# Optimization experiments

Hardware: AMD Instinct MI355X
Metric: run time of the kernel (lower is better)

Reference implementation:

```python
import jax, jax.numpy as jnp
import numpy as np
from jax import lax

NUM_LAYERS = 2
H = 1024   # per-direction hidden = state_size / 2
IN = 768   # BERT hidden size == input_size
SEQ = 1024


def _init_params(key):
    ks = jax.random.split(key, 4 * NUM_LAYERS * 2)
    mk = lambda k, shape: jax.random.normal(k, shape, jnp.float32) * 0.02
    out = {}
    i = 0
    for d in ("fw", "bw"):
        for l in range(NUM_LAYERS):
            ins = IN if l == 0 else H
            out[f"{d}{l}_Wih"] = mk(ks[i], (4 * H, ins)); i += 1
            out[f"{d}{l}_Whh"] = mk(ks[i], (4 * H, H)); i += 1
            out[f"{d}{l}_bih"] = mk(ks[i], (4 * H,)); i += 1
            out[f"{d}{l}_bhh"] = mk(ks[i], (4 * H,)); i += 1
    return out


def setup_inputs() -> dict:
    key = jax.random.key(0)
    kx, kp = jax.random.split(key)
    inp = {"last_hidden": jax.random.normal(kx, (1, SEQ, IN), jnp.float32)}
    inp.update(_init_params(kp))
    return inp


def _run_direction(x, params):
    """x: [S, in_dim]; params: list of (Wih, Whh, bih, bhh) per layer.
    Stacked LSTMCells (torch gate order i,f,g,o), dropout_amount=0."""
    def step(carry, xt):
        new = []
        inp = xt
        for (h, c), (Wih, Whh, bih, bhh) in zip(carry, params):
            gates = Wih @ inp + bih + Whh @ h + bhh  # [4H]
            i, f, g, o = jnp.split(gates, 4)
            c = jax.nn.sigmoid(f) * c + jax.nn.sigmoid(i) * jnp.tanh(g)
            h = jax.nn.sigmoid(o) * jnp.tanh(c)
            new.append((h, c))
            inp = h
        return tuple(new), inp  # output = top layer h
    init = tuple((jnp.zeros((H,), x.dtype), jnp.zeros((H,), x.dtype)) for _ in params)
    final, outs = lax.scan(step, init, x)
    cs = jnp.stack([c for (_, c) in final])  # [L, H] final cell states
    hs = jnp.stack([h for (h, _) in final])  # [L, H] final hidden states
    return cs, hs, outs                      # outs: [S, H]


def reference(last_hidden, fw0_Wih, fw0_Whh, fw0_bih, fw0_bhh,
              fw1_Wih, fw1_Whh, fw1_bih, fw1_bhh,
              bw0_Wih, bw0_Whh, bw0_bih, bw0_bhh,
              bw1_Wih, bw1_Whh, bw1_bih, bw1_bhh):
    x = last_hidden[0]  # squeeze batch of 1 -> [S, IN]
    fw = [(fw0_Wih, fw0_Whh, fw0_bih, fw0_bhh), (fw1_Wih, fw1_Whh, fw1_bih, fw1_bhh)]
    bw = [(bw0_Wih, bw0_Whh, bw0_bih, bw0_bhh), (bw1_Wih, bw1_Whh, bw1_bih, bw1_bhh)]
    f_c, f_h, f_out = _run_direction(x, fw)
    b_c, b_h, b_out = _run_direction(x[::-1], bw)
    b_out = b_out[::-1]  # re-align backward outputs with token order
    cell_memories = jnp.concatenate([f_c, b_c], axis=1)      # [L, 2H]
    hidden_states = jnp.concatenate([f_h, b_h], axis=1)      # [L, 2H]
    final_outputs = jnp.concatenate([f_out, b_out], axis=1)  # [S, 2H]
    return cell_memories, hidden_states, final_outputs
```

## Files before the change

kernel.cpp:

```cpp
#include <hip/hip_runtime.h>

typedef unsigned int u32;
typedef unsigned short u16;
typedef unsigned long long u64;
typedef __attribute__((ext_vector_type(8))) short v8s;
typedef __attribute__((ext_vector_type(4))) float v4f;

#define VALIDMASK 0x0001000100010001ULL

__device__ __forceinline__ float bf2f(u16 v) { return __uint_as_float(((u32)v) << 16); }
__device__ __forceinline__ u16 f2bf(float f) {
    u32 u = __float_as_uint(f);
    return (u16)((u + 0x7fffu + ((u >> 16) & 1u)) >> 16);
}
__device__ __forceinline__ u32 f2bfo(float f) { return (__float_as_uint(f) >> 16) | 1u; }
__device__ __forceinline__ float sigf(float x) { return 1.0f / (1.0f + __expf(-x)); }
__device__ __forceinline__ float tanhfast(float x) {
    float e = __expf(2.0f * x);
    return 1.0f - 2.0f / (e + 1.0f);
}
__device__ __forceinline__ v8s pack8(v4f a, v4f b) {
    v8s r;
    r[0] = (short)f2bf(a[0]); r[1] = (short)f2bf(a[1]);
    r[2] = (short)f2bf(a[2]); r[3] = (short)f2bf(a[3]);
    r[4] = (short)f2bf(b[0]); r[5] = (short)f2bf(b[1]);
    r[6] = (short)f2bf(b[2]); r[7] = (short)f2bf(b[3]);
    return r;
}

__global__ __launch_bounds__(256) void gemm_ih(
    const float* __restrict__ A, const float* __restrict__ W,
    const float* __restrict__ bih, const float* __restrict__ bhh,
    u16* __restrict__ out, int K)
{
    __shared__ u16 As[128][40];
    __shared__ u16 Bs[128][40];
    const int tm = blockIdx.x, tn = blockIdx.y;
    const int tid = threadIdx.x;
    const int lane = tid & 63;
    const int wv = tid >> 6;
    const int wm = wv >> 1, wn = wv & 1;
    const int fr = lane & 15, fq = lane >> 4;

    v4f acc[4][4] = {};

    for (int kt = 0; kt < K; kt += 32) {
#pragma unroll
        for (int it = 0; it < 2; ++it) {
            int q = tid + it * 256;
            int r = q >> 2;
            int c8 = (q & 3) * 8;
            const float* pa = &A[(size_t)(tm * 128 + r) * K + kt + c8];
            const float* pw = &W[(size_t)(tn * 128 + r) * K + kt + c8];
            *(v8s*)&As[r][c8] = pack8(*(const v4f*)pa, *(const v4f*)(pa + 4));
            *(v8s*)&Bs[r][c8] = pack8(*(const v4f*)pw, *(const v4f*)(pw + 4));
        }
        __syncthreads();
        v8s af[4], bfr[4];
#pragma unroll
        for (int mi = 0; mi < 4; ++mi)
            af[mi] = *(const v8s*)&As[wm * 64 + mi * 16 + fr][fq * 8];
#pragma unroll
        for (int ni = 0; ni < 4; ++ni)
            bfr[ni] = *(const v8s*)&Bs[wn * 64 + ni * 16 + fr][fq * 8];
#pragma unroll
        for (int mi = 0; mi < 4; ++mi)
#pragma unroll
            for (int ni = 0; ni < 4; ++ni)
                acc[mi][ni] = __builtin_amdgcn_mfma_f32_16x16x32_bf16(af[mi], bfr[ni], acc[mi][ni], 0, 0, 0);
        __syncthreads();
    }

#pragma unroll
    for (int ni = 0; ni < 4; ++ni) {
        int col = tn * 128 + wn * 64 + ni * 16 + fr;
        float bias = bih[col] + bhh[col];
#pragma unroll
        for (int mi = 0; mi < 4; ++mi)
#pragma unroll
            for (int j = 0; j < 4; ++j) {
                int row = tm * 128 + wm * 64 + mi * 16 + fq * 4 + j;
                out[(size_t)row * 4096 + col] = f2bf(acc[mi][ni][j] + bias);
            }
    }
}

__global__ __launch_bounds__(64, 1) void lstm_fused(
    const float* __restrict__ fw0_Whh, const float* __restrict__ bw0_Whh,
    const float* __restrict__ fw1_Whh, const float* __restrict__ bw1_Whh,
    const float* __restrict__ fw1_Wih, const float* __restrict__ bw1_Wih,
    const float* __restrict__ fw1_bih, const float* __restrict__ fw1_bhh,
    const float* __restrict__ bw1_bih, const float* __restrict__ bw1_bhh,
    const u16*  __restrict__ precomp0,
    u64* htag0,
    u64* htag1,
    float* __restrict__ out)
{
    extern __shared__ char smem[];
    char* hA = smem + 65536;
    char* hB = smem + 65536 + 2048;
    float* gd = (float*)(smem + 65536 + 4096);

    const int lane = threadIdx.x;
    const int bid = blockIdx.x;
    const int role = bid >> 8;
    const int sub = bid & 255;
    const int d = sub >> 7;
    const int wg = sub & 127;
    const int e0 = wg << 3;

    const float* __restrict__ Whh =
        role ? (d ? bw1_Whh : fw1_Whh) : (d ? bw0_Whh : fw0_Whh);

    v8s awf0[32], awf1[32];
    {
        int r0 = lane & 15, r1 = r0 + 16;
        int kq = (lane >> 4) << 3;
        const float* q0 = &Whh[(size_t)((r0 >> 3) * 1024 + e0 + (r0 & 7)) * 1024 + kq];
        const float* q1 = &Whh[(size_t)((r1 >> 3) * 1024 + e0 + (r1 & 7)) * 1024 + kq];
#pragma unroll
        for (int c = 0; c < 32; ++c) {
            awf0[c] = pack8(*(const v4f*)(q0 + 32 * c), *(const v4f*)(q0 + 32 * c + 4));
            awf1[c] = pack8(*(const v4f*)(q1 + 32 * c), *(const v4f*)(q1 + 32 * c + 4));
        }
    }

    float bias_i = 0.f, bias_f = 0.f, bias_g = 0.f, bias_o = 0.f;
    if (role) {
        const float* __restrict__ Wih = d ? bw1_Wih : fw1_Wih;
        for (int i = 0; i < 64; ++i) {
            int q = lane + (i << 6);
            int row = q >> 7;
            int kb = (q & 127) << 4;
            const float* p = &Wih[(size_t)((row >> 3) * 1024 + e0 + (row & 7)) * 1024 + (kb >> 1)];
            int addr = (row << 11) + kb;
            addr ^= ((row & 7) << 4);
            *(v8s*)(smem + addr) = pack8(*(const v4f*)p, *(const v4f*)(p + 4));
        }
        if (lane < 8) {
            const float* bi = d ? bw1_bih : fw1_bih;
            const float* bh = d ? bw1_bhh : fw1_bhh;
            bias_i = bi[e0 + lane]        + bh[e0 + lane];
            bias_f = bi[1024 + e0 + lane] + bh[1024 + e0 + lane];
            bias_g = bi[2048 + e0 + lane] + bh[2048 + e0 + lane];
            bias_o = bi[3072 + e0 + lane] + bh[3072 + e0 + lane];
        }
    }

    u64* hown = (role ? htag1 : htag0) + (size_t)d * 1024 * 256;
    u64* hin  = htag0 + (size_t)d * 1024 * 256;
    float* cm_out = out + role * 2048;
    float* hs_out = out + 4096 + role * 2048;
    float* seq_out = out + 8192;

    float c_state = 0.0f;

    for (int s = 0; s < 1024; ++s) {
        v4f acc0 = {0.f, 0.f, 0.f, 0.f}, acc1 = {0.f, 0.f, 0.f, 0.f};

        u16 ri = 0, rf = 0, rg = 0, ro = 0;
        if (!role && lane < 8) {
            int sx = d ? (1023 - s) : s;
            const u16* pr = precomp0 + ((size_t)d * 1024 + sx) * 4096 + e0 + lane;
            ri = pr[0]; rf = pr[1024]; rg = pr[2048]; ro = pr[3072];
        }

        if (role) {
            u64* p = hin + (size_t)s * 256 + (lane << 2);
            u64 a, b, c2, d2;
            for (;;) {
                a  = __hip_atomic_load(&p[0], __ATOMIC_RELAXED, __HIP_MEMORY_SCOPE_AGENT);
                b  = __hip_atomic_load(&p[1], __ATOMIC_RELAXED, __HIP_MEMORY_SCOPE_AGENT);
                c2 = __hip_atomic_load(&p[2], __ATOMIC_RELAXED, __HIP_MEMORY_SCOPE_AGENT);
                d2 = __hip_atomic_load(&p[3], __ATOMIC_RELAXED, __HIP_MEMORY_SCOPE_AGENT);
                if ((((a & b) & (c2 & d2)) & VALIDMASK) == VALIDMASK) break;
                __builtin_amdgcn_s_sleep(1);
            }
            *(u64*)(hB + (lane << 5))      = a;
            *(u64*)(hB + (lane << 5) + 8)  = b;
            *(u64*)(hB + (lane << 5) + 16) = c2;
            *(u64*)(hB + (lane << 5) + 24) = d2;
            asm volatile("s_waitcnt lgkmcnt(0)" ::: "memory");
            int r0 = lane & 15;
            int sw = (r0 & 7) << 4;
#pragma unroll
            for (int c = 0; c < 32; ++c) {
                int kb = (c << 6) + ((lane >> 4) << 4);
                v8s bfr = *(const v8s*)(hB + kb);
                v8s a0 = *(const v8s*)(smem + (((r0 << 11) + kb) ^ sw));
                v8s a1 = *(const v8s*)(smem + ((((r0 + 16) << 11) + kb) ^ sw));
                acc0 = __builtin_amdgcn_mfma_f32_16x16x32_bf16(a0, bfr, acc0, 0, 0, 0);
                acc1 = __builtin_amdgcn_mfma_f32_16x16x32_bf16(a1, bfr, acc1, 0, 0, 0);
            }
        }

        if (s > 0) {
            u64* p = hown + (size_t)(s - 1) * 256 + (lane << 2);
            u64 a, b, c2, d2;
            for (;;) {
                a  = __hip_atomic_load(&p[0], __ATOMIC_RELAXED, __HIP_MEMORY_SCOPE_AGENT);
                b  = __hip_atomic_load(&p[1], __ATOMIC_RELAXED, __HIP_MEMORY_SCOPE_AGENT);
                c2 = __hip_atomic_load(&p[2], __ATOMIC_RELAXED, __HIP_MEMORY_SCOPE_AGENT);
                d2 = __hip_atomic_load(&p[3], __ATOMIC_RELAXED, __HIP_MEMORY_SCOPE_AGENT);
                if ((((a & b) & (c2 & d2)) & VALIDMASK) == VALIDMASK) break;
                __builtin_amdgcn_s_sleep(1);
            }
            *(u64*)(hA + (lane << 5))      = a;
            *(u64*)(hA + (lane << 5) + 8)  = b;
            *(u64*)(hA + (lane << 5) + 16) = c2;
            *(u64*)(hA + (lane << 5) + 24) = d2;
            asm volatile("s_waitcnt lgkmcnt(0)" ::: "memory");
#pragma unroll
            for (int c = 0; c < 32; ++c) {
                v8s bfr = *(const v8s*)(hA + (c << 6) + ((lane >> 4) << 4));
                acc0 = __builtin_amdgcn_mfma_f32_16x16x32_bf16(awf0[c], bfr, acc0, 0, 0, 0);
                acc1 = __builtin_amdgcn_mfma_f32_16x16x32_bf16(awf1[c], bfr, acc1, 0, 0, 0);
            }
        }

        if ((lane & 15) == 0) {
            int rbase = (lane >> 4) << 2;
            *(v4f*)&gd[rbase]      = acc0;
            *(v4f*)&gd[16 + rbase] = acc1;
        }
        asm volatile("s_waitcnt lgkmcnt(0)" ::: "memory");

        float h_new = 0.0f;
        if (lane < 8) {
            float Gi = gd[lane]      + (role ? bias_i : bf2f(ri));
            float Gf = gd[8 + lane]  + (role ? bias_f : bf2f(rf));
            float Gg = gd[16 + lane] + (role ? bias_g : bf2f(rg));
            float Go = gd[24 + lane] + (role ? bias_o : bf2f(ro));
            c_state = sigf(Gf) * c_state + sigf(Gi) * tanhfast(Gg);
            h_new = sigf(Go) * tanhfast(c_state);
        }

        u32 w0 = f2bfo(__shfl(h_new, (lane << 2)))     | (f2bfo(__shfl(h_new, (lane << 2) + 1)) << 16);
        u32 w1 = f2bfo(__shfl(h_new, (lane << 2) + 2)) | (f2bfo(__shfl(h_new, (lane << 2) + 3)) << 16);
        if (lane < 2) {
            u64 val = ((u64)w1 << 32) | w0;
            __hip_atomic_store(&hown[(size_t)s * 256 + (e0 >> 2) + lane], val,
                               __ATOMIC_RELAXED, __HIP_MEMORY_SCOPE_AGENT);
        }

        if (lane < 8) {
            if (role) {
                int rrow = d ? (1023 - s) : s;
                seq_out[(size_t)rrow * 2048 + d * 1024 + e0 + lane] = h_new;
            }
            if (s == 1023) {
                cm_out[d * 1024 + e0 + lane] = c_state;
                hs_out[d * 1024 + e0 + lane] = h_new;
            }
        }
    }
}

extern "C" void kernel_launch(void* const* d_in, const int* in_sizes, int n_in,
                              void* d_out, int out_size, void* d_ws, size_t ws_size,
                              hipStream_t stream) {
    (void)in_sizes; (void)n_in; (void)out_size; (void)ws_size;

    const float* x       = (const float*)d_in[0];
    const float* fw0_Wih = (const float*)d_in[1];
    const float* fw0_Whh = (const float*)d_in[2];
    const float* fw0_bih = (const float*)d_in[3];
    const float* fw0_bhh = (const float*)d_in[4];
    const float* fw1_Wih = (const float*)d_in[5];
    const float* fw1_Whh = (const float*)d_in[6];
    const float* fw1_bih = (const float*)d_in[7];
    const float* fw1_bhh = (const float*)d_in[8];
    const float* bw0_Wih = (const float*)d_in[9];
    const float* bw0_Whh = (const float*)d_in[10];
    const float* bw0_bih = (const float*)d_in[11];
    const float* bw0_bhh = (const float*)d_in[12];
    const float* bw1_Wih = (const float*)d_in[13];
    const float* bw1_Whh = (const float*)d_in[14];
    const float* bw1_bih = (const float*)d_in[15];
    const float* bw1_bhh = (const float*)d_in[16];

    char* ws = (char*)d_ws;
    u16* precomp = (u16*)ws;
    u64* htag0   = (u64*)(ws + (16 << 20));
    u64* htag1   = (u64*)(ws + (20 << 20));
    float* out   = (float*)d_out;

    hipMemsetAsync(htag0, 0, (size_t)8 << 20, stream);

    dim3 g(8, 32);
    gemm_ih<<<g, 256, 0, stream>>>(x, fw0_Wih, fw0_bih, fw0_bhh, precomp, 768);
    gemm_ih<<<g, 256, 0, stream>>>(x, bw0_Wih, bw0_bih, bw0_bhh,
                                   precomp + (size_t)1024 * 4096, 768);

    lstm_fused<<<512, 64, 69760, stream>>>(
        fw0_Whh, bw0_Whh, fw1_Whh, bw1_Whh, fw1_Wih, bw1_Wih,
        fw1_bih, fw1_bhh, bw1_bih, bw1_bhh,
        precomp, htag0, htag1, out);
}
```

Before: 3.430 ms.

## Relayout LDS weight tile, coalesce h polling, split MFMA accumulators, raise priority

Rearranges the layer-1 input-weight tile in shared memory into a fragment-major, conflict-free layout so each lane reads contiguous 16-byte chunks without the XOR swizzle. The hidden-state polling loads change from four consecutive words per lane to strided words across lanes, which coalesces the global reads, and the LDS staging is changed to match. The MFMA chains are split into two independent accumulator pairs to shorten dependency chains. s_setprio raises wave priority during the matmul section. The risk is that the new LDS layout introduces bank conflicts, and the extra accumulator registers add pressure next to the 64 register-resident weight fragments.

```diff
diff --git a/kernel.cpp b/kernel.cpp
--- a/kernel.cpp
+++ b/kernel.cpp
@@ -108,6 +108,7 @@
     const int d = sub >> 7;
     const int wg = sub & 127;
     const int e0 = wg << 3;
+    const int q16 = (lane >> 4) << 4;
 
     const float* __restrict__ Whh =
         role ? (d ? bw1_Whh : fw1_Whh) : (d ? bw0_Whh : fw0_Whh);
@@ -116,26 +117,27 @@
     {
         int r0 = lane & 15, r1 = r0 + 16;
         int kq = (lane >> 4) << 3;
-        const float* q0 = &Whh[(size_t)((r0 >> 3) * 1024 + e0 + (r0 & 7)) * 1024 + kq];
-        const float* q1 = &Whh[(size_t)((r1 >> 3) * 1024 + e0 + (r1 & 7)) * 1024 + kq];
+        const float* p0 = &Whh[(size_t)((r0 >> 3) * 1024 + e0 + (r0 & 7)) * 1024 + kq];
+        const float* p1 = &Whh[(size_t)((r1 >> 3) * 1024 + e0 + (r1 & 7)) * 1024 + kq];
 #pragma unroll
         for (int c = 0; c < 32; ++c) {
-            awf0[c] = pack8(*(const v4f*)(q0 + 32 * c), *(const v4f*)(q0 + 32 * c + 4));
-            awf1[c] = pack8(*(const v4f*)(q1 + 32 * c), *(const v4f*)(q1 + 32 * c + 4));
+            awf0[c] = pack8(*(const v4f*)(p0 + 32 * c), *(const v4f*)(p0 + 32 * c + 4));
+            awf1[c] = pack8(*(const v4f*)(p1 + 32 * c), *(const v4f*)(p1 + 32 * c + 4));
         }
     }
 
     float bias_i = 0.f, bias_f = 0.f, bias_g = 0.f, bias_o = 0.f;
     if (role) {
         const float* __restrict__ Wih = d ? bw1_Wih : fw1_Wih;
-        for (int i = 0; i < 64; ++i) {
-            int q = lane + (i << 6);
-            int row = q >> 7;
-            int kb = (q & 127) << 4;
-            const float* p = &Wih[(size_t)((row >> 3) * 1024 + e0 + (row & 7)) * 1024 + (kb >> 1)];
-            int addr = (row << 11) + kb;
-            addr ^= ((row & 7) << 4);
-            *(v8s*)(smem + addr) = pack8(*(const v4f*)p, *(const v4f*)(p + 4));
+        for (int i = 0; i < 32; ++i) {
+            const float* prow = &Wih[(size_t)((i >> 3) * 1024 + e0 + (i & 7)) * 1024];
+            int base = ((lane & 3) << 9) + ((i >> 4) << 8) + ((i & 15) << 4);
+            const float* p0 = prow + lane * 8;
+            const float* p1 = prow + 512 + lane * 8;
+            *(v8s*)(smem + ((lane >> 2) << 11) + base) =
+                pack8(*(const v4f*)p0, *(const v4f*)(p0 + 4));
+            *(v8s*)(smem + ((16 + (lane >> 2)) << 11) + base) =
+                pack8(*(const v4f*)p1, *(const v4f*)(p1 + 4));
         }
         if (lane < 8) {
             const float* bi = d ? bw1_bih : fw1_bih;
@@ -156,7 +158,8 @@
     float c_state = 0.0f;
 
     for (int s = 0; s < 1024; ++s) {
-        v4f acc0 = {0.f, 0.f, 0.f, 0.f}, acc1 = {0.f, 0.f, 0.f, 0.f};
+        v4f acc0a = {0.f,0.f,0.f,0.f}, acc0b = {0.f,0.f,0.f,0.f};
+        v4f acc1a = {0.f,0.f,0.f,0.f}, acc1b = {0.f,0.f,0.f,0.f};
 
         u16 ri = 0, rf = 0, rg = 0, ro = 0;
         if (!role && lane < 8) {
@@ -166,58 +169,70 @@
         }
 
         if (role) {
-            u64* p = hin + (size_t)s * 256 + (lane << 2);
+            u64* p = hin + (size_t)s * 256 + lane;
             u64 a, b, c2, d2;
             for (;;) {
-                a  = __hip_atomic_load(&p[0], __ATOMIC_RELAXED, __HIP_MEMORY_SCOPE_AGENT);
-                b  = __hip_atomic_load(&p[1], __ATOMIC_RELAXED, __HIP_MEMORY_SCOPE_AGENT);
-                c2 = __hip_atomic_load(&p[2], __ATOMIC_RELAXED, __HIP_MEMORY_SCOPE_AGENT);
-                d2 = __hip_atomic_load(&p[3], __ATOMIC_RELAXED, __HIP_MEMORY_SCOPE_AGENT);
+                a  = __hip_atomic_load(&p[0],   __ATOMIC_RELAXED, __HIP_MEMORY_SCOPE_AGENT);
+                b  = __hip_atomic_load(&p[64],  __ATOMIC_RELAXED, __HIP_MEMORY_SCOPE_AGENT);
+                c2 = __hip_atomic_load(&p[128], __ATOMIC_RELAXED, __HIP_MEMORY_SCOPE_AGENT);
+                d2 = __hip_atomic_load(&p[192], __ATOMIC_RELAXED, __HIP_MEMORY_SCOPE_AGENT);
                 if ((((a & b) & (c2 & d2)) & VALIDMASK) == VALIDMASK) break;
                 __builtin_amdgcn_s_sleep(1);
             }
-            *(u64*)(hB + (lane << 5))      = a;
-            *(u64*)(hB + (lane << 5) + 8)  = b;
-            *(u64*)(hB + (lane << 5) + 16) = c2;
-            *(u64*)(hB + (lane << 5) + 24) = d2;
+            __builtin_amdgcn_s_setprio(1);
+            *(u64*)(hB + (lane << 3))        = a;
+            *(u64*)(hB + (lane << 3) + 512)  = b;
+            *(u64*)(hB + (lane << 3) + 1024) = c2;
+            *(u64*)(hB + (lane << 3) + 1536) = d2;
             asm volatile("s_waitcnt lgkmcnt(0)" ::: "memory");
-            int r0 = lane & 15;
-            int sw = (r0 & 7) << 4;
-#pragma unroll
-            for (int c = 0; c < 32; ++c) {
-                int kb = (c << 6) + ((lane >> 4) << 4);
-                v8s bfr = *(const v8s*)(hB + kb);
-                v8s a0 = *(const v8s*)(smem + (((r0 << 11) + kb) ^ sw));
-                v8s a1 = *(const v8s*)(smem + ((((r0 + 16) << 11) + kb) ^ sw));
-                acc0 = __builtin_amdgcn_mfma_f32_16x16x32_bf16(a0, bfr, acc0, 0, 0, 0);
-                acc1 = __builtin_amdgcn_mfma_f32_16x16x32_bf16(a1, bfr, acc1, 0, 0, 0);
-            }
+            const int fb = ((lane >> 4) << 9) + ((lane & 15) << 4);
+#pragma unroll
+            for (int c = 0; c < 32; c += 2) {
+                v8s b0 = *(const v8s*)(hB + (c << 6) + q16);
+                v8s b1 = *(const v8s*)(hB + ((c + 1) << 6) + q16);
+                v8s a00 = *(const v8s*)(smem + (c << 11) + fb);
+                v8s a01 = *(const v8s*)(smem + (c << 11) + fb + 256);
+                v8s a10 = *(const v8s*)(smem + ((c + 1) << 11) + fb);
+                v8s a11 = *(const v8s*)(smem + ((c + 1) << 11) + fb + 256);
+                acc0a = __builtin_amdgcn_mfma_f32_16x16x32_bf16(a00, b0, acc0a, 0, 0, 0);
+                acc1a = __builtin_amdgcn_mfma_f32_16x16x32_bf16(a01, b0, acc1a, 0, 0, 0);
+                acc0b = __builtin_amdgcn_mfma_f32_16x16x32_bf16(a10, b1, acc0b, 0, 0, 0);
+                acc1b = __builtin_amdgcn_mfma_f32_16x16x32_bf16(a11, b1, acc1b, 0, 0, 0);
+            }
+            __builtin_amdgcn_s_setprio(0);
         }
 
         if (s > 0) {
-            u64* p = hown + (size_t)(s - 1) * 256 + (lane << 2);
+            u64* p = hown + (size_t)(s - 1) * 256 + lane;
             u64 a, b, c2, d2;
             for (;;) {
-                a  = __hip_atomic_load(&p[0], __ATOMIC_RELAXED, __HIP_MEMORY_SCOPE_AGENT);
-                b  = __hip_atomic_load(&p[1], __ATOMIC_RELAXED, __HIP_MEMORY_SCOPE_AGENT);
-                c2 = __hip_atomic_load(&p[2], __ATOMIC_RELAXED, __HIP_MEMORY_SCOPE_AGENT);
-                d2 = __hip_atomic_load(&p[3], __ATOMIC_RELAXED, __HIP_MEMORY_SCOPE_AGENT);
+                a  = __hip_atomic_load(&p[0],   __ATOMIC_RELAXED, __HIP_MEMORY_SCOPE_AGENT);
+                b  = __hip_atomic_load(&p[64],  __ATOMIC_RELAXED, __HIP_MEMORY_SCOPE_AGENT);
+                c2 = __hip_atomic_load(&p[128], __ATOMIC_RELAXED, __HIP_MEMORY_SCOPE_AGENT);
+                d2 = __hip_atomic_load(&p[192], __ATOMIC_RELAXED, __HIP_MEMORY_SCOPE_AGENT);
                 if ((((a & b) & (c2 & d2)) & VALIDMASK) == VALIDMASK) break;
                 __builtin_amdgcn_s_sleep(1);
             }
-            *(u64*)(hA + (lane << 5))      = a;
-            *(u64*)(hA + (lane << 5) + 8)  = b;
-            *(u64*)(hA + (lane << 5) + 16) = c2;
-            *(u64*)(hA + (lane << 5) + 24) = d2;
+            __builtin_amdgcn_s_setprio(1);
+            *(u64*)(hA + (lane << 3))        = a;
+            *(u64*)(hA + (lane << 3) + 512)  = b;
+            *(u64*)(hA + (lane << 3) + 1024) = c2;
+            *(u64*)(hA + (lane << 3) + 1536) = d2;
             asm volatile("s_waitcnt lgkmcnt(0)" ::: "memory");
 #pragma unroll
-            for (int c = 0; c < 32; ++c) {
-                v8s bfr = *(const v8s*)(hA + (c << 6) + ((lane >> 4) << 4));
-                acc0 = __builtin_amdgcn_mfma_f32_16x16x32_bf16(awf0[c], bfr, acc0, 0, 0, 0);
-                acc1 = __builtin_amdgcn_mfma_f32_16x16x32_bf16(awf1[c], bfr, acc1, 0, 0, 0);
-            }
-        }
-
+            for (int c = 0; c < 32; c += 2) {
+                v8s b0 = *(const v8s*)(hA + (c << 6) + q16);
+                v8s b1 = *(const v8s*)(hA + ((c + 1) << 6) + q16);
+                acc0a = __builtin_amdgcn_mfma_f32_16x16x32_bf16(awf0[c], b0, acc0a, 0, 0, 0);
+                acc1a = __builtin_amdgcn_mfma_f32_16x16x32_bf16(awf1[c], b0, acc1a, 0, 0, 0);
+                acc0b = __builtin_amdgcn_mfma_f32_16x16x32_bf16(awf0[c + 1], b1, acc0b, 0, 0, 0);
+                acc1b = __builtin_amdgcn_mfma_f32_16x16x32_bf16(awf1[c + 1], b1, acc1b, 0, 0, 0);
+            }
+            __builtin_amdgcn_s_setprio(0);
+        }
+
+        v4f acc0 = acc0a + acc0b;
+        v4f acc1 = acc1a + acc1b;
         if ((lane & 15) == 0) {
             int rbase = (lane >> 4) << 2;
             *(v4f*)&gd[rbase]      = acc0;
```

Result: slower. 3.623 ms (+5.6%).
